# Kernel tuning notes

Hardware: AMD Instinct MI355X
Metric: run time of the kernel (lower is better)

## Reference

```python
import jax, jax.numpy as jnp
import numpy as np

N = 100000        # nodes per batch
B = 1             # batch_size
E = 3200000       # edges
IN_F = 128        # in_features
ATT = 128         # attention_dim
HEADS = 8
DK = ATT // HEADS
SLOPE = 0.2       # leaky_relu_slope


def setup_inputs() -> dict:
    key = jax.random.key(0)
    k1, k2, k3, k4 = jax.random.split(key, 4)
    x = jax.random.normal(k1, (B * N, IN_F), dtype=jnp.float32)
    edge = jax.random.randint(k2, (B, 2, E), 0, N)
    # xavier_normal with gain=1.414 on W:[IN_F, ATT]
    W = jax.random.normal(k3, (IN_F, ATT), dtype=jnp.float32) * (1.414 * np.sqrt(2.0 / (IN_F + ATT)))
    # a originally [1, 2*d_k, 1, 1]; flattened to [2*d_k] (same math)
    a = jax.random.normal(k4, (2 * DK,), dtype=jnp.float32) * (1.414 * np.sqrt(2.0 / (2 * DK + 1)))
    return {"x": x, "edge": edge, "W": W, "a": a}


def _segment_softmax(scores, seg):
    # scores: [E, H], seg: [E] -> softmax within each segment (node id)
    smax = jax.ops.segment_max(scores, seg, num_segments=N)
    ex = jnp.exp(scores - smax[seg])
    denom = jax.ops.segment_sum(ex, seg, num_segments=N)
    return ex / denom[seg]


def reference(x, edge, W, a):
    wx = x @ W                                           # [B*N, ATT]
    h = wx.reshape(B, N, HEADS, DK).transpose(0, 1, 3, 2)  # [B, N, DK, H]
    a1, a2 = a[:DK], a[DK:]
    # sum(a * concat(h_src, h_dst)) = a1.h_src + a2.h_dst (linearity)
    s_src = jnp.einsum('bnkh,k->bnh', h, a1)             # [B, N, H]
    s_dst = jnp.einsum('bnkh,k->bnh', h, a2)             # [B, N, H]
    src = edge[:, 0, :]                                  # [B, E]
    dst = edge[:, 1, :]                                  # [B, E]
    gather = jax.vmap(lambda s, i: s[i])
    scores = gather(s_src, src) + gather(s_dst, dst)     # [B, E, H]
    edge_e = jnp.where(scores > 0, scores, SLOPE * scores)  # leaky relu
    # attention_norm_idx = 0 -> normalize over edges sharing a source node
    attention = jax.vmap(_segment_softmax)(edge_e, src)  # [B, E, H]
    return attention, wx
```

## Files before the change

### kernel.cpp

```cpp
#include <hip/hip_runtime.h>
#include <hip/hip_fp16.h>

#define N_NODES 100000
#define E_EDGES 3200000
#define IN_F 128
#define ATT 128
#define HEADS 8
#define DK 16
#define SLOPE 0.2f
#define NH (N_NODES * HEADS)

#define CHUNK 224
#define NBINS 448
#define NS 4
#define HB 512
#define EPB 6272

static __device__ __forceinline__ void h8_to_f(const __half* p, float* o)
{
    const float4 raw = *(const float4*)p;
    const __half2* h2 = (const __half2*)&raw;
#pragma unroll
    for (int k = 0; k < 4; k++) {
        const float2 f = __half22float2(h2[k]);
        o[2 * k]     = f.x;
        o[2 * k + 1] = f.y;
    }
}

static __device__ __forceinline__ unsigned short f_to_b(float f)
{
    unsigned int u = __float_as_uint(f);
    u += 0x7FFFu + ((u >> 16) & 1u);
    return (unsigned short)(u >> 16);
}

static __device__ __forceinline__ void b8_to_f(const unsigned short* p, float* o)
{
    const uint4 raw = *(const uint4*)p;
    const unsigned int u[4] = {raw.x, raw.y, raw.z, raw.w};
#pragma unroll
    for (int k = 0; k < 4; k++) {
        o[2 * k]     = __uint_as_float(u[k] << 16);
        o[2 * k + 1] = __uint_as_float(u[k] & 0xFFFF0000u);
    }
}

__global__ __launch_bounds__(256) void gemm_s_kernel(
    const float* __restrict__ x, const float* __restrict__ W,
    const float* __restrict__ a, float* __restrict__ wx,
    __half* __restrict__ s_src16, __half* __restrict__ s_dst16)
{
    __shared__ float xs[8][128];
    __shared__ float Ws[8][128];

    const int tid = threadIdx.x;
    const int ty  = tid >> 4;
    const int tx  = tid & 15;
    const int row0 = blockIdx.x * 128;

    float acc[8][8];
#pragma unroll
    for (int i = 0; i < 8; i++)
#pragma unroll
        for (int j = 0; j < 8; j++) acc[i][j] = 0.f;

    const int lrow  = tid >> 1;
    const int khalf = (tid & 1) * 4;
    const int wkk   = tid >> 5;
    const int wc    = (tid & 31) * 4;

    for (int k0 = 0; k0 < IN_F; k0 += 8) {
        float4 xv = make_float4(0.f, 0.f, 0.f, 0.f);
        const int grow = row0 + lrow;
        if (grow < N_NODES)
            xv = *(const float4*)(x + (size_t)grow * IN_F + k0 + khalf);
        const float4 wv = *(const float4*)(W + (size_t)(k0 + wkk) * ATT + wc);

        __syncthreads();
        xs[khalf + 0][lrow] = xv.x;
        xs[khalf + 1][lrow] = xv.y;
        xs[khalf + 2][lrow] = xv.z;
        xs[khalf + 3][lrow] = xv.w;
        *(float4*)(&Ws[wkk][wc]) = wv;
        __syncthreads();

#pragma unroll
        for (int kk = 0; kk < 8; kk++) {
            float av[8], bv[8];
            *(float4*)(av)     = *(const float4*)(&xs[kk][ty * 8]);
            *(float4*)(av + 4) = *(const float4*)(&xs[kk][ty * 8 + 4]);
            *(float4*)(bv)     = *(const float4*)(&Ws[kk][tx * 8]);
            *(float4*)(bv + 4) = *(const float4*)(&Ws[kk][tx * 8 + 4]);
#pragma unroll
            for (int r = 0; r < 8; r++)
#pragma unroll
                for (int c = 0; c < 8; c++)
                    acc[r][c] = fmaf(av[r], bv[c], acc[r][c]);
        }
    }

    const int koff = (tx & 1) * 8;
    const int head = tx >> 1;
    float a1[8], a2[8];
#pragma unroll
    for (int c = 0; c < 8; c++) {
        a1[c] = a[koff + c];
        a2[c] = a[DK + koff + c];
    }

#pragma unroll
    for (int r = 0; r < 8; r++) {
        const int grow = row0 + ty * 8 + r;
        const bool ok = (grow < N_NODES);
        if (ok) {
            *(float4*)(wx + (size_t)grow * ATT + tx * 8) =
                make_float4(acc[r][0], acc[r][1], acc[r][2], acc[r][3]);
            *(float4*)(wx + (size_t)grow * ATT + tx * 8 + 4) =
                make_float4(acc[r][4], acc[r][5], acc[r][6], acc[r][7]);
        }
        float p1 = 0.f, p2 = 0.f;
#pragma unroll
        for (int c = 0; c < 8; c++) {
            p1 = fmaf(acc[r][c], a1[c], p1);
            p2 = fmaf(acc[r][c], a2[c], p2);
        }
        p1 += __shfl_xor(p1, 1);
        p2 += __shfl_xor(p2, 1);
        if (((tx & 1) == 0) && ok) {
            s_src16[(size_t)grow * HEADS + head] = __float2half_rn(p1);
            s_dst16[(size_t)grow * HEADS + head] = __float2half_rn(p2);
        }
    }
}

__global__ __launch_bounds__(256) void hist_kernel(
    const int* __restrict__ src, int* __restrict__ counts)
{
    __shared__ int h[NBINS];
    const int t = threadIdx.x;
    const int b = blockIdx.x;
    for (int i = t; i < NBINS; i += 256) h[i] = 0;
    __syncthreads();

    const int rb = b * EPB;
    const int re = min(rb + EPB, E_EDGES);
    for (int i = rb + t * 4; i < re; i += 256 * 4) {
        const int4 s4 = *(const int4*)(src + i);
        atomicAdd(&h[s4.x / CHUNK], 1);
        atomicAdd(&h[s4.y / CHUNK], 1);
        atomicAdd(&h[s4.z / CHUNK], 1);
        atomicAdd(&h[s4.w / CHUNK], 1);
    }
    __syncthreads();
    for (int i = t; i < NBINS; i += 256) counts[i * HB + b] = h[i];
}

__global__ __launch_bounds__(1024) void scan_kernel(
    const int* __restrict__ counts, int* __restrict__ offs)
{
    __shared__ int part[1024];
    const int t = threadIdx.x;
    const int per = (NBINS * HB) / 1024;
    const int base = t * per;

    int sum = 0;
    for (int i = 0; i < per; i++) sum += counts[base + i];
    part[t] = sum;
    __syncthreads();

    for (int off = 1; off < 1024; off <<= 1) {
        int v = 0;
        if (t >= off) v = part[t - off];
        __syncthreads();
        if (t >= off) part[t] += v;
        __syncthreads();
    }

    int run = (t == 0) ? 0 : part[t - 1];
    for (int i = 0; i < per; i++) {
        offs[base + i] = run;
        run += counts[base + i];
    }
}

__global__ __launch_bounds__(256) void scatter_kernel(
    const int* __restrict__ src, const int* __restrict__ dst,
    const int* __restrict__ offs, unsigned int* __restrict__ binned)
{
    __shared__ int cur[NBINS];
    const int t = threadIdx.x;
    const int b = blockIdx.x;
    for (int i = t; i < NBINS; i += 256) cur[i] = offs[i * HB + b];
    __syncthreads();

    const int rb = b * EPB;
    const int re = min(rb + EPB, E_EDGES);
    for (int i = rb + t * 4; i < re; i += 256 * 4) {
        const int4 s4 = *(const int4*)(src + i);
        const int4 d4 = *(const int4*)(dst + i);
        const int ss[4] = {s4.x, s4.y, s4.z, s4.w};
        const int dd[4] = {d4.x, d4.y, d4.z, d4.w};
#pragma unroll
        for (int j = 0; j < 4; j++) {
            const int c = ss[j] / CHUNK;
            const int pos = atomicAdd(&cur[c], 1);
            binned[pos] = ((unsigned int)(ss[j] - c * CHUNK) << 17) |
                          (unsigned int)dd[j];
        }
    }
}

__global__ __launch_bounds__(256, 8) void denom_binned_kernel(
    const unsigned int* __restrict__ binned, const int* __restrict__ offs,
    const __half* __restrict__ s_src16, const __half* __restrict__ s_dst16,
    float* __restrict__ denoms)
{
    __shared__ float acc[HEADS][CHUNK + 1];
    __shared__ float ssrc[CHUNK * HEADS];

    const int t  = threadIdx.x;
    const int c  = blockIdx.x;
    const int j  = blockIdx.y;
    const int lo = c * CHUNK;
    const int hi = min(lo + CHUNK, N_NODES);

    for (int i = t; i < HEADS * (CHUNK + 1); i += 256)
        ((float*)acc)[i] = 0.f;
    {
        for (int nd = t; nd < hi - lo; nd += 256) {
            float f[8];
            h8_to_f(s_src16 + (size_t)(lo + nd) * HEADS, f);
            float4* dp = (float4*)(ssrc + nd * HEADS);
            dp[0] = make_float4(f[0], f[1], f[2], f[3]);
            dp[1] = make_float4(f[4], f[5], f[6], f[7]);
        }
    }
    __syncthreads();

    const int start = offs[c * HB];
    const int end   = (c + 1 < NBINS) ? offs[(c + 1) * HB] : E_EDGES;
    const int len   = end - start;
    const int e0 = start + (int)((long long)len * j / NS);
    const int e1 = start + (int)((long long)len * (j + 1) / NS);

    int i = e0 + t;
    bool v0 = i < e1;
    bool v1 = i + 256 < e1;
    unsigned int pw0 = v0 ? binned[i] : 0u;
    unsigned int pw1 = v1 ? binned[i + 256] : 0u;

    while (v0) {
        const unsigned int w0 = pw0;
        const unsigned int w1 = v1 ? pw1 : pw0;
        const bool cv1 = v1;

        i += 512;
        v0 = i < e1;
        v1 = i + 256 < e1;
        if (v0) pw0 = binned[i];
        if (v1) pw1 = binned[i + 256];

        const int sl0 = (int)(w0 >> 17), di0 = (int)(w0 & 0x1FFFFu);
        const int sl1 = (int)(w1 >> 17), di1 = (int)(w1 & 0x1FFFFu);

        float db0[8], db1[8];
        h8_to_f(s_dst16 + (size_t)di0 * HEADS, db0);
        h8_to_f(s_dst16 + (size_t)di1 * HEADS, db1);

        const float4* qs0 = (const float4*)(ssrc + sl0 * HEADS);
        const float4* qs1 = (const float4*)(ssrc + sl1 * HEADS);
        const float4 xa0 = qs0[0], xa1 = qs0[1];
        const float4 ya0 = qs1[0], ya1 = qs1[1];
        const float sa[8] = {xa0.x, xa0.y, xa0.z, xa0.w, xa1.x, xa1.y, xa1.z, xa1.w};
        const float sb[8] = {ya0.x, ya0.y, ya0.z, ya0.w, ya1.x, ya1.y, ya1.z, ya1.w};

#pragma unroll
        for (int h = 0; h < 8; h++) {
            float v = sa[h] + db0[h]; v = v > 0.f ? v : SLOPE * v;
            atomicAdd(&acc[h][sl0], __expf(v));
        }
        if (cv1) {
#pragma unroll
            for (int h = 0; h < 8; h++) {
                float v = sb[h] + db1[h]; v = v > 0.f ? v : SLOPE * v;
                atomicAdd(&acc[h][sl1], __expf(v));
            }
        }
    }
    __syncthreads();

    float* outp = denoms + (size_t)j * NH + (size_t)lo * HEADS;
    for (int nd = t; nd < hi - lo; nd += 256) {
        const float4 o0 = make_float4(acc[0][nd], acc[1][nd], acc[2][nd], acc[3][nd]);
        const float4 o1 = make_float4(acc[4][nd], acc[5][nd], acc[6][nd], acc[7][nd]);
        *(float4*)(outp + (size_t)nd * 8)     = o0;
        *(float4*)(outp + (size_t)nd * 8 + 4) = o1;
    }
}

__global__ __launch_bounds__(256) void reduce_recip_kernel(
    const float* __restrict__ denoms, unsigned short* __restrict__ rdb)
{
    const int i = blockIdx.x * 256 + threadIdx.x;
    if (i >= NH) return;
    float s = 0.f;
#pragma unroll
    for (int c = 0; c < NS; c++) s += denoms[(size_t)c * NH + i];
    rdb[i] = f_to_b(__frcp_rn(s));
}

__global__ __launch_bounds__(256) void norm_e_kernel(
    const int* __restrict__ src, const int* __restrict__ dst,
    const __half* __restrict__ s_src16, const __half* __restrict__ s_dst16,
    const unsigned short* __restrict__ rdb, float* __restrict__ att)
{
    const int e0 = (blockIdx.x * 256 + threadIdx.x) * 2;
    if (e0 >= E_EDGES) return;
    const int2 sp = *(const int2*)(src + e0);
    const int2 dp = *(const int2*)(dst + e0);

    float sa[8], sb[8], d0[8], d1[8], r0[8], r1[8];
    h8_to_f(s_src16 + (size_t)sp.x * HEADS, sa);
    h8_to_f(s_src16 + (size_t)sp.y * HEADS, sb);
    h8_to_f(s_dst16 + (size_t)dp.x * HEADS, d0);
    h8_to_f(s_dst16 + (size_t)dp.y * HEADS, d1);
    b8_to_f(rdb + (size_t)sp.x * HEADS, r0);
    b8_to_f(rdb + (size_t)sp.y * HEADS, r1);

    float o0[8], o1[8];
#pragma unroll
    for (int h = 0; h < 8; h++) {
        float v = sa[h] + d0[h]; v = v > 0.f ? v : SLOPE * v;
        o0[h] = __expf(v) * r0[h];
        float u = sb[h] + d1[h]; u = u > 0.f ? u : SLOPE * u;
        o1[h] = __expf(u) * r1[h];
    }

    float4* pa = (float4*)(att + (size_t)e0 * HEADS);
    pa[0] = make_float4(o0[0], o0[1], o0[2], o0[3]);
    pa[1] = make_float4(o0[4], o0[5], o0[6], o0[7]);
    pa[2] = make_float4(o1[0], o1[1], o1[2], o1[3]);
    pa[3] = make_float4(o1[4], o1[5], o1[6], o1[7]);
}

extern "C" void kernel_launch(void* const* d_in, const int* in_sizes, int n_in,
                              void* d_out, int out_size, void* d_ws, size_t ws_size,
                              hipStream_t stream)
{
    const float* x    = (const float*)d_in[0];
    const int*   edge = (const int*)d_in[1];
    const float* W    = (const float*)d_in[2];
    const float* a    = (const float*)d_in[3];

    float* out = (float*)d_out;
    float* att = out;
    float* wx  = out + (size_t)E_EDGES * HEADS;

    float*  ws      = (float*)d_ws;
    float*  denoms  = ws;
    __half* s_src16 = (__half*)(denoms + (size_t)NS * NH);
    __half* s_dst16 = s_src16 + (size_t)NH;
    unsigned short* rdb = (unsigned short*)(s_dst16 + (size_t)NH);
    int*    counts  = (int*)(rdb + (size_t)NH);
    int*    offs    = counts + (size_t)NBINS * HB;
    unsigned int* binned = (unsigned int*)(offs + (size_t)NBINS * HB);

    const int* src = edge;
    const int* dst = edge + E_EDGES;

    const int gemm_blocks = (N_NODES + 127) / 128;
    gemm_s_kernel<<<gemm_blocks, 256, 0, stream>>>(x, W, a, wx, s_src16, s_dst16);

    hist_kernel<<<HB, 256, 0, stream>>>(src, counts);
    scan_kernel<<<1, 1024, 0, stream>>>(counts, offs);
    scatter_kernel<<<HB, 256, 0, stream>>>(src, dst, offs, binned);

    dim3 bgrid(NBINS, NS);
    denom_binned_kernel<<<bgrid, 256, 0, stream>>>(binned, offs, s_src16, s_dst16, denoms);

    const int nblocks = (NH + 255) / 256;
    reduce_recip_kernel<<<nblocks, 256, 0, stream>>>(denoms, rdb);

    const int eblocks = (E_EDGES / 2 + 255) / 256;
    norm_e_kernel<<<eblocks, 256, 0, stream>>>(src, dst, s_src16, s_dst16,
                                               rdb, att);
}
```

Before: 578.7 us.

## Fuse denominator reduction and reciprocal into binned kernel, interleave src scores with reciprocals

The denominator kernel now processes each source chunk in a single 512-thread block instead of four split blocks. It computes the bf16 reciprocal directly, which removes the partial-denominator buffer and the separate reduce kernel. Source scores and reciprocal denominators are packed into one 32-byte record per node, so the per-edge normalization kernel does one contiguous gather instead of two scattered ones. Histogram blocks are halved with twice the edges per block. The cost is fewer, larger blocks in the denominator pass (448 blocks), which may leave CUs idle or unbalanced across chunks.

```diff
diff --git a/kernel.cpp b/kernel.cpp
--- a/kernel.cpp
+++ b/kernel.cpp
@@ -12,9 +12,9 @@
 
 #define CHUNK 224
 #define NBINS 448
-#define NS 4
-#define HB 512
-#define EPB 6272
+#define HB 256
+#define EPB 12544
+#define DTH 512
 
 static __device__ __forceinline__ void h8_to_f(const __half* p, float* o)
 {
@@ -28,16 +28,15 @@
     }
 }
 
-static __device__ __forceinline__ unsigned short f_to_b(float f)
+static __device__ __forceinline__ unsigned int f_to_b(float f)
 {
     unsigned int u = __float_as_uint(f);
     u += 0x7FFFu + ((u >> 16) & 1u);
-    return (unsigned short)(u >> 16);
-}
-
-static __device__ __forceinline__ void b8_to_f(const unsigned short* p, float* o)
-{
-    const uint4 raw = *(const uint4*)p;
+    return u >> 16;
+}
+
+static __device__ __forceinline__ void b8_dec(const uint4 raw, float* o)
+{
     const unsigned int u[4] = {raw.x, raw.y, raw.z, raw.w};
 #pragma unroll
     for (int k = 0; k < 4; k++) {
@@ -46,10 +45,11 @@
     }
 }
 
+
 __global__ __launch_bounds__(256) void gemm_s_kernel(
     const float* __restrict__ x, const float* __restrict__ W,
     const float* __restrict__ a, float* __restrict__ wx,
-    __half* __restrict__ s_src16, __half* __restrict__ s_dst16)
+    __half* __restrict__ combo, __half* __restrict__ s_dst16)
 {
     __shared__ float xs[8][128];
     __shared__ float Ws[8][128];
@@ -128,7 +128,7 @@
         p1 += __shfl_xor(p1, 1);
         p2 += __shfl_xor(p2, 1);
         if (((tx & 1) == 0) && ok) {
-            s_src16[(size_t)grow * HEADS + head] = __float2half_rn(p1);
+            combo[(size_t)grow * 16 + head]      = __float2half_rn(p1);
             s_dst16[(size_t)grow * HEADS + head] = __float2half_rn(p2);
         }
     }
@@ -211,26 +211,24 @@
     }
 }
 
-__global__ __launch_bounds__(256, 8) void denom_binned_kernel(
+__global__ __launch_bounds__(DTH) void denom_binned_kernel(
     const unsigned int* __restrict__ binned, const int* __restrict__ offs,
-    const __half* __restrict__ s_src16, const __half* __restrict__ s_dst16,
-    float* __restrict__ denoms)
+    __half* __restrict__ combo, const __half* __restrict__ s_dst16)
 {
     __shared__ float acc[HEADS][CHUNK + 1];
     __shared__ float ssrc[CHUNK * HEADS];
 
     const int t  = threadIdx.x;
     const int c  = blockIdx.x;
-    const int j  = blockIdx.y;
     const int lo = c * CHUNK;
     const int hi = min(lo + CHUNK, N_NODES);
 
-    for (int i = t; i < HEADS * (CHUNK + 1); i += 256)
+    for (int i = t; i < HEADS * (CHUNK + 1); i += DTH)
         ((float*)acc)[i] = 0.f;
     {
-        for (int nd = t; nd < hi - lo; nd += 256) {
+        for (int nd = t; nd < hi - lo; nd += DTH) {
             float f[8];
-            h8_to_f(s_src16 + (size_t)(lo + nd) * HEADS, f);
+            h8_to_f(combo + (size_t)(lo + nd) * 16, f);
             float4* dp = (float4*)(ssrc + nd * HEADS);
             dp[0] = make_float4(f[0], f[1], f[2], f[3]);
             dp[1] = make_float4(f[4], f[5], f[6], f[7]);
@@ -238,28 +236,25 @@
     }
     __syncthreads();
 
-    const int start = offs[c * HB];
-    const int end   = (c + 1 < NBINS) ? offs[(c + 1) * HB] : E_EDGES;
-    const int len   = end - start;
-    const int e0 = start + (int)((long long)len * j / NS);
-    const int e1 = start + (int)((long long)len * (j + 1) / NS);
+    const int e0 = offs[c * HB];
+    const int e1 = (c + 1 < NBINS) ? offs[(c + 1) * HB] : E_EDGES;
 
     int i = e0 + t;
     bool v0 = i < e1;
-    bool v1 = i + 256 < e1;
+    bool v1 = i + DTH < e1;
     unsigned int pw0 = v0 ? binned[i] : 0u;
-    unsigned int pw1 = v1 ? binned[i + 256] : 0u;
+    unsigned int pw1 = v1 ? binned[i + DTH] : 0u;
 
     while (v0) {
         const unsigned int w0 = pw0;
         const unsigned int w1 = v1 ? pw1 : pw0;
         const bool cv1 = v1;
 
-        i += 512;
+        i += 2 * DTH;
         v0 = i < e1;
-        v1 = i + 256 < e1;
+        v1 = i + DTH < e1;
         if (v0) pw0 = binned[i];
-        if (v1) pw1 = binned[i + 256];
+        if (v1) pw1 = binned[i + DTH];
 
         const int sl0 = (int)(w0 >> 17), di0 = (int)(w0 & 0x1FFFFu);
         const int sl1 = (int)(w1 >> 17), di1 = (int)(w1 & 0x1FFFFu);
@@ -290,43 +285,42 @@
     }
     __syncthreads();
 
-    float* outp = denoms + (size_t)j * NH + (size_t)lo * HEADS;
-    for (int nd = t; nd < hi - lo; nd += 256) {
-        const float4 o0 = make_float4(acc[0][nd], acc[1][nd], acc[2][nd], acc[3][nd]);
-        const float4 o1 = make_float4(acc[4][nd], acc[5][nd], acc[6][nd], acc[7][nd]);
-        *(float4*)(outp + (size_t)nd * 8)     = o0;
-        *(float4*)(outp + (size_t)nd * 8 + 4) = o1;
-    }
-}
-
-__global__ __launch_bounds__(256) void reduce_recip_kernel(
-    const float* __restrict__ denoms, unsigned short* __restrict__ rdb)
-{
-    const int i = blockIdx.x * 256 + threadIdx.x;
-    if (i >= NH) return;
-    float s = 0.f;
-#pragma unroll
-    for (int c = 0; c < NS; c++) s += denoms[(size_t)c * NH + i];
-    rdb[i] = f_to_b(__frcp_rn(s));
+    for (int nd = t; nd < hi - lo; nd += DTH) {
+        unsigned int u[4];
+#pragma unroll
+        for (int k = 0; k < 4; k++) {
+            const unsigned int b0 = f_to_b(__frcp_rn(acc[2 * k][nd]));
+            const unsigned int b1 = f_to_b(__frcp_rn(acc[2 * k + 1][nd]));
+            u[k] = b0 | (b1 << 16);
+        }
+        *(uint4*)(combo + (size_t)(lo + nd) * 16 + 8) =
+            make_uint4(u[0], u[1], u[2], u[3]);
+    }
 }
 
 __global__ __launch_bounds__(256) void norm_e_kernel(
     const int* __restrict__ src, const int* __restrict__ dst,
-    const __half* __restrict__ s_src16, const __half* __restrict__ s_dst16,
-    const unsigned short* __restrict__ rdb, float* __restrict__ att)
+    const __half* __restrict__ combo, const __half* __restrict__ s_dst16,
+    float* __restrict__ att)
 {
     const int e0 = (blockIdx.x * 256 + threadIdx.x) * 2;
     if (e0 >= E_EDGES) return;
     const int2 sp = *(const int2*)(src + e0);
     const int2 dp = *(const int2*)(dst + e0);
 
-    float sa[8], sb[8], d0[8], d1[8], r0[8], r1[8];
-    h8_to_f(s_src16 + (size_t)sp.x * HEADS, sa);
-    h8_to_f(s_src16 + (size_t)sp.y * HEADS, sb);
+    const uint4* c0 = (const uint4*)(combo + (size_t)sp.x * 16);
+    const uint4* c1 = (const uint4*)(combo + (size_t)sp.y * 16);
+    const uint4 c0s = c0[0], c0r = c0[1];
+    const uint4 c1s = c1[0], c1r = c1[1];
+    float d0[8], d1[8];
     h8_to_f(s_dst16 + (size_t)dp.x * HEADS, d0);
     h8_to_f(s_dst16 + (size_t)dp.y * HEADS, d1);
-    b8_to_f(rdb + (size_t)sp.x * HEADS, r0);
-    b8_to_f(rdb + (size_t)sp.y * HEADS, r1);
+
+    float sa[8], sb[8], r0[8], r1[8];
+    h8_to_f((const __half*)&c0s, sa);
+    h8_to_f((const __half*)&c1s, sb);
+    b8_dec(c0r, r0);
+    b8_dec(c1r, r1);
 
     float o0[8], o1[8];
 #pragma unroll
@@ -357,12 +351,9 @@
     float* att = out;
     float* wx  = out + (size_t)E_EDGES * HEADS;
 
-    float*  ws      = (float*)d_ws;
-    float*  denoms  = ws;
-    __half* s_src16 = (__half*)(denoms + (size_t)NS * NH);
-    __half* s_dst16 = s_src16 + (size_t)NH;
-    unsigned short* rdb = (unsigned short*)(s_dst16 + (size_t)NH);
-    int*    counts  = (int*)(rdb + (size_t)NH);
+    __half* combo   = (__half*)d_ws;
+    __half* s_dst16 = combo + (size_t)N_NODES * 16;
+    int*    counts  = (int*)(s_dst16 + (size_t)NH);
     int*    offs    = counts + (size_t)NBINS * HB;
     unsigned int* binned = (unsigned int*)(offs + (size_t)NBINS * HB);
 
@@ -370,19 +361,14 @@
     const int* dst = edge + E_EDGES;
 
     const int gemm_blocks = (N_NODES + 127) / 128;
-    gemm_s_kernel<<<gemm_blocks, 256, 0, stream>>>(x, W, a, wx, s_src16, s_dst16);
+    gemm_s_kernel<<<gemm_blocks, 256, 0, stream>>>(x, W, a, wx, combo, s_dst16);
 
     hist_kernel<<<HB, 256, 0, stream>>>(src, counts);
     scan_kernel<<<1, 1024, 0, stream>>>(counts, offs);
     scatter_kernel<<<HB, 256, 0, stream>>>(src, dst, offs, binned);
 
-    dim3 bgrid(NBINS, NS);
-    denom_binned_kernel<<<bgrid, 256, 0, stream>>>(binned, offs, s_src16, s_dst16, denoms);
-
-    const int nblocks = (NH + 255) / 256;
-    reduce_recip_kernel<<<nblocks, 256, 0, stream>>>(denoms, rdb);
+    denom_binned_kernel<<<NBINS, DTH, 0, stream>>>(binned, offs, combo, s_dst16);
 
     const int eblocks = (E_EDGES / 2 + 255) / 256;
-    norm_e_kernel<<<eblocks, 256, 0, stream>>>(src, dst, s_src16, s_dst16,
-                                               rdb, att);
-}
+    norm_e_kernel<<<eblocks, 256, 0, stream>>>(src, dst, combo, s_dst16, att);
+}
```

After: 533.2 us. 1.09x faster.
